# Optimization experiments

Measured on AMD Instinct MI355X. Metric: run time of the kernel, lower is better.

## Reference

```python
import jax, jax.numpy as jnp
import numpy as np

FORMULA_OH_SIZES = [20, 20, 20, 20, 20]
SPECT_BIN_N = 512


def layer_norm(x, g, b, eps=1e-5):
    m = jnp.mean(x, axis=-1, keepdims=True)
    v = jnp.var(x, axis=-1, keepdims=True)
    return (x - m) * jax.lax.rsqrt(v + eps) * g + b


def gru_cell(x, h, W_ih, W_hh, b_ih, b_hh):
    # torch.nn.GRUCell math
    gi = x @ W_ih.T + b_ih
    gh = h @ W_hh.T + b_hh
    i_r, i_z, i_n = jnp.split(gi, 3, axis=-1)
    h_r, h_z, h_n = jnp.split(gh, 3, axis=-1)
    r = jax.nn.sigmoid(i_r + h_r)
    z = jax.nn.sigmoid(i_z + h_z)
    n = jnp.tanh(i_n + r * h_n)
    return (1.0 - z) * n + z * h


def structured_one_hot(x, sizes, accum=True):
    # x: [N, len(sizes)] integer element counts -> concatenated (accumulated) one-hots
    outs = []
    for i, s in enumerate(sizes):
        v = jnp.clip(x[:, i].astype(jnp.int32), 0, s - 1)
        if accum:
            oh = (jnp.arange(s)[None, :] <= v[:, None]).astype(jnp.float32)  # thermometer
        else:
            oh = jax.nn.one_hot(v, s, dtype=jnp.float32)
        outs.append(oh)
    return jnp.concatenate(outs, axis=-1)


def setup_inputs():
    key = jax.random.key(0)
    ks = jax.random.split(key, 16)
    B, A, GF, HW, S, M = 16, 32, 128, 4, 4096, 8
    G = GF * HW                       # 512 = g_feat_in * highway_steps_n
    FE = sum(FORMULA_OH_SIZES)        # 100
    D = 512                           # internal_d
    vert_feat_in = jax.random.normal(ks[0], (B, A, GF, HW), jnp.float32)
    vert_mask_in = jnp.ones((B, A), jnp.float32)
    elem_id = jax.random.randint(ks[1], (B, A), 0, 5)
    vert_element_oh = jax.nn.one_hot(elem_id, 5, dtype=jnp.float32)
    adj_oh = jnp.zeros((B, A, A, 4), jnp.float32)  # unused by forward
    atom_subsets = jax.random.bernoulli(ks[2], 0.5, (B, S, A)).astype(jnp.float32)
    masses = jax.random.uniform(ks[3], (B, S, M), jnp.float32, 0.0, SPECT_BIN_N - 1.0)
    intens = jax.random.uniform(ks[4], (B, S, M), jnp.float32)
    atom_subsets_peaks = jnp.stack([masses, intens], axis=-1)

    def lin(k, o, i):
        return (jax.random.normal(k, (o, i), jnp.float32) / np.sqrt(i)).astype(jnp.float32)

    return dict(
        vert_feat_in=vert_feat_in, vert_mask_in=vert_mask_in,
        vert_element_oh=vert_element_oh, adj_oh=adj_oh,
        atom_subsets=atom_subsets, atom_subsets_peaks=atom_subsets_peaks,
        ln_sub_g=jnp.ones((G,), jnp.float32), ln_sub_b=jnp.zeros((G,), jnp.float32),
        W_ih=lin(ks[5], 3 * G, FE), W_hh=lin(ks[6], 3 * G, G),
        b_ih=jnp.zeros((3 * G,), jnp.float32), b_hh=jnp.zeros((3 * G,), jnp.float32),
        W1=lin(ks[7], D, G), b1=jnp.zeros((D,), jnp.float32),
        W2a=lin(ks[8], D, D), b2a=jnp.zeros((D,), jnp.float32),
        W2b=lin(ks[9], D, D), b2b=jnp.zeros((D,), jnp.float32),
        ln_pre_g=jnp.ones((D,), jnp.float32), ln_pre_b=jnp.zeros((D,), jnp.float32),
        Ws=lin(ks[10], 1, D), bs=jnp.zeros((1,), jnp.float32),
    )


def reference(vert_feat_in, vert_mask_in, vert_element_oh, adj_oh, atom_subsets,
              atom_subsets_peaks, ln_sub_g, ln_sub_b, W_ih, W_hh, b_ih, b_hh,
              W1, b1, W2a, b2a, W2b, b2b, ln_pre_g, ln_pre_b, Ws, bs):
    B, A, GF, HW = vert_feat_in.shape
    S = atom_subsets.shape[1]
    vf = vert_feat_in.reshape(B, A, GF * HW)                       # [B,A,G]
    masked_vf = vf * vert_mask_in[:, :, None]
    subs_m = atom_subsets * vert_mask_in[:, None, :]               # [B,S,A]
    swvs = jnp.einsum('bag,bsa->bsg', masked_vf, subs_m)           # [B,S,G]
    # per-subset element counts -> structured one-hot formula encoding
    counts = jnp.einsum('bae,bsa->bse', vert_element_oh, atom_subsets).astype(jnp.int32)
    pf_flat = structured_one_hot(counts.reshape(B * S, -1), FORMULA_OH_SIZES, accum=True)
    subset_size = jnp.sum(subs_m, axis=2) + 1e-4                   # [B,S]
    mean = swvs / subset_size[:, :, None]
    normed = layer_norm(mean, ln_sub_g, ln_sub_b)                  # [B,S,G]
    h = gru_cell(pf_flat, normed.reshape(B * S, -1), W_ih, W_hh, b_ih, b_hh)
    h = h.reshape(normed.shape)
    x = jax.nn.relu(h @ W1.T + b1)
    x = jax.nn.relu(x @ W2a.T + b2a)
    x = jax.nn.relu(x @ W2b.T + b2b)   # (extra F.relu in original is idempotent)
    x = layer_norm(x, ln_pre_g, ln_pre_b)
    scores = (x @ Ws.T + bs)[..., 0]                               # [B,S]
    probs = jax.nn.softmax(scores, axis=-1)
    # mass histogram: scatter intensity*prob into rounded-mass bins
    masses = atom_subsets_peaks[..., 0]                            # [B,S,M]
    intens = atom_subsets_peaks[..., 1]
    bins = jnp.clip(jnp.round(masses).astype(jnp.int32), 0, SPECT_BIN_N - 1)
    contrib = intens * probs[:, :, None]                           # [B,S,M]
    spect = jnp.zeros((B, SPECT_BIN_N), x.dtype).at[
        jnp.arange(B)[:, None], bins.reshape(B, -1)].add(contrib.reshape(B, -1))
    return (spect, probs)
```

## Files before the change

### kernel.cpp

```cpp
#include <hip/hip_runtime.h>
#include <math.h>

#define B_ 16
#define A_ 32
#define G_ 512
#define S_ 4096
#define M_ 8
#define BS_ 65536
#define KC_ 640
#define NG_ 1536
#define SMH 16384

typedef _Float16 half8 __attribute__((ext_vector_type(8)));
typedef _Float16 half4v __attribute__((ext_vector_type(4)));
typedef _Float16 half2v __attribute__((ext_vector_type(2)));
typedef float floatx4 __attribute__((ext_vector_type(4)));

typedef const __attribute__((address_space(1))) void* gas_t;
typedef __attribute__((address_space(3))) void* las_t;

__device__ __forceinline__ float wave_sum_f(float v){
#pragma unroll
  for (int o = 32; o > 0; o >>= 1) v += __shfl_xor(v, o);
  return v;
}
__device__ __forceinline__ float wave_max_f(float v){
#pragma unroll
  for (int o = 32; o > 0; o >>= 1) v = fmaxf(v, __shfl_xor(v, o));
  return v;
}
__device__ __forceinline__ float sigmoidf_(float x){ return 1.f/(1.f+__expf(-x)); }
__device__ __forceinline__ float tanhf_(float x){ return 1.f - 2.f/(__expf(2.f*x)+1.f); }

__global__ __launch_bounds__(256) void k_cvt3(const float* __restrict__ s0,
                                              const float* __restrict__ s1,
                                              const float* __restrict__ s2,
                                              _Float16* __restrict__ d){
  const float* s = (blockIdx.y == 0) ? s0 : (blockIdx.y == 1) ? s1 : s2;
  int i = (blockIdx.x*256 + threadIdx.x)*4;
  if (i >= G_*G_) return;
  float4 v = *(const float4*)(s+i);
  half4v o; o[0]=(_Float16)v.x; o[1]=(_Float16)v.y; o[2]=(_Float16)v.z; o[3]=(_Float16)v.w;
  *(half4v*)(d + (size_t)blockIdx.y*G_*G_ + i) = o;
}

__global__ __launch_bounds__(64) void k_buildw(const float* __restrict__ Whh,
                                               const float* __restrict__ Wih,
                                               _Float16* __restrict__ Wcat){
  int j = blockIdx.x;
  for (int p = threadIdx.x; p < KC_; p += 64){
    float v = 0.f;
    if (p < 512) v = Whh[(size_t)j*512 + p];
    else if (p < 612) v = Wih[(size_t)j*100 + (p - 512)];
    Wcat[(size_t)j*KC_ + p] = (_Float16)v;
  }
}

__global__ __launch_bounds__(256) void k_prep_mfma(
    const float* __restrict__ vf, const float* __restrict__ mask,
    const float* __restrict__ eoh, const float* __restrict__ subs,
    const float* __restrict__ ln_g, const float* __restrict__ ln_b,
    _Float16* __restrict__ Abuf){
  __shared__ _Float16 s_mvfT[G_*A_];
  __shared__ _Float16 s_sm[128*A_];
  __shared__ float s_m[A_];
  __shared__ float s_e[A_*5];
  __shared__ float s_ssum[128];
  __shared__ float s_red1[2][4][16];
  __shared__ float s_red2[2][4][16];
  int tid = threadIdx.x;
  int bx = blockIdx.x, b = blockIdx.y;
  int lane = tid & 63, w = tid >> 6;
  int q = lane >> 4, l15 = lane & 15;
  size_t row0 = (size_t)b*S_ + (size_t)bx*128;
  if (tid < A_)   s_m[tid] = mask[b*A_ + tid];
  if (tid < A_*5) s_e[tid] = eoh[b*A_*5 + tid];
  __syncthreads();
  {
    int p = tid & 15, gseg = tid >> 4;
    float mk0 = s_m[2*p], mk1 = s_m[2*p+1];
    const float* v0 = vf + ((size_t)b*A_ + 2*p)*G_ + gseg*32;
    const float* v1 = v0 + G_;
#pragma unroll
    for (int i = 0; i < 32; i += 4){
      float4 a = *(const float4*)(v0 + i);
      float4 c = *(const float4*)(v1 + i);
      float av[4] = {a.x, a.y, a.z, a.w};
      float cv[4] = {c.x, c.y, c.z, c.w};
#pragma unroll
      for (int j = 0; j < 4; ++j){
        half2v h; h[0] = (_Float16)(av[j]*mk0); h[1] = (_Float16)(cv[j]*mk1);
        *(half2v*)(s_mvfT + (gseg*32 + i + j)*A_ + 2*p) = h;
      }
    }
  }
  {
    int s = tid >> 1, hh = tid & 1;
    const float* sp = subs + (row0 + s)*A_ + hh*16;
    _Float16* dst = s_sm + s*A_ + hh*16;
#pragma unroll
    for (int i = 0; i < 16; i += 4){
      float4 v = *(const float4*)(sp + i);
      half4v h; h[0]=(_Float16)v.x; h[1]=(_Float16)v.y; h[2]=(_Float16)v.z; h[3]=(_Float16)v.w;
      *(half4v*)(dst + i) = h;
    }
  }
  __syncthreads();
  if (tid < 128){
    int s = tid;
    float ssum = 0.f, c0=0.f, c1=0.f, c2=0.f, c3=0.f, c4=0.f;
#pragma unroll
    for (int a = 0; a < A_; ++a){
      float v = (float)s_sm[s*A_ + a];
      ssum += v * s_m[a];
      c0 += v * s_e[a*5+0]; c1 += v * s_e[a*5+1]; c2 += v * s_e[a*5+2];
      c3 += v * s_e[a*5+3]; c4 += v * s_e[a*5+4];
    }
    int cc[5];
    cc[0] = min(max((int)(c0+0.5f),0),19); cc[1] = min(max((int)(c1+0.5f),0),19);
    cc[2] = min(max((int)(c2+0.5f),0),19); cc[3] = min(max((int)(c3+0.5f),0),19);
    cc[4] = min(max((int)(c4+0.5f),0),19);
    s_ssum[s] = ssum;
    _Float16* dst = Abuf + (row0 + s)*KC_ + 512;
#pragma unroll
    for (int t = 0; t < 16; ++t){
      half8 hv;
#pragma unroll
      for (int u = 0; u < 8; ++u){
        int k = t*8 + u;
        float v = 0.f;
        if (k < 100){ int f = k/20, l = k - f*20; v = (l <= cc[f]) ? 1.f : 0.f; }
        hv[u] = (_Float16)v;
      }
      *(half8*)(dst + t*8) = hv;
    }
  }
  half8 bf[8]; float lng[8], lnb[8];
#pragma unroll
  for (int t = 0; t < 8; ++t){
    int g = w*128 + t*16 + l15;
    bf[t] = *(const half8*)(s_mvfT + g*A_ + q*8);
    lng[t] = ln_g[g]; lnb[t] = ln_b[g];
  }
  __syncthreads();
  for (int gi = 0; gi < 8; ++gi){
    half8 af = *(const half8*)(s_sm + (gi*16 + l15)*A_ + q*8);
    floatx4 c[8];
#pragma unroll
    for (int t = 0; t < 8; ++t){
      floatx4 z = {0.f, 0.f, 0.f, 0.f};
      c[t] = __builtin_amdgcn_mfma_f32_16x16x32_f16(af, bf[t], z, 0, 0, 0);
    }
    float p1[4] = {0.f,0.f,0.f,0.f}, p2[4] = {0.f,0.f,0.f,0.f};
#pragma unroll
    for (int t = 0; t < 8; ++t)
#pragma unroll
      for (int r = 0; r < 4; ++r){ float v = c[t][r]; p1[r] += v; p2[r] += v*v; }
#pragma unroll
    for (int off = 1; off < 16; off <<= 1)
#pragma unroll
      for (int r = 0; r < 4; ++r){
        p1[r] += __shfl_xor(p1[r], off);
        p2[r] += __shfl_xor(p2[r], off);
      }
    int gb = gi & 1;
    if (l15 == 0){
#pragma unroll
      for (int r = 0; r < 4; ++r){ s_red1[gb][w][q*4+r] = p1[r]; s_red2[gb][w][q*4+r] = p2[r]; }
    }
    __syncthreads();
#pragma unroll
    for (int r = 0; r < 4; ++r){
      int sl = gi*16 + q*4 + r;
      int rr = q*4 + r;
      float t1 = s_red1[gb][0][rr] + s_red1[gb][1][rr] + s_red1[gb][2][rr] + s_red1[gb][3][rr];
      float t2 = s_red2[gb][0][rr] + s_red2[gb][1][rr] + s_red2[gb][2][rr] + s_red2[gb][3][rr];
      float inv = 1.f/(s_ssum[sl] + 1e-4f);
      float mu = t1*inv*(1.f/512.f);
      float var = t2*inv*inv*(1.f/512.f) - mu*mu;
      float rs = rsqrtf(var + 1e-5f);
      _Float16* orow = Abuf + (row0 + sl)*KC_;
#pragma unroll
      for (int t = 0; t < 8; ++t){
        float o = (c[t][r]*inv - mu)*rs*lng[t] + lnb[t];
        orow[w*128 + t*16 + l15] = (_Float16)o;
      }
    }
  }
}

#define GSTG_A(T) do{ \
    __builtin_amdgcn_global_load_lds((gas_t)(qA0 + (T)*64),            (las_t)(&gmA[(T)&1][0] + wvid*1024),        16, 0, 0); \
    __builtin_amdgcn_global_load_lds((gas_t)(qA1 + (T)*64),            (las_t)(&gmA[(T)&1][0] + wvid*1024 + 512),  16, 0, 0); \
    __builtin_amdgcn_global_load_lds((gas_t)(qA0 + 128*KC_ + (T)*64),  (las_t)(&gmA[(T)&1][0] + 8192 + wvid*1024), 16, 0, 0); \
    __builtin_amdgcn_global_load_lds((gas_t)(qA1 + 128*KC_ + (T)*64),  (las_t)(&gmA[(T)&1][0] + 8192 + wvid*1024 + 512), 16, 0, 0); \
  }while(0)
#define GSTG_B(T) do{ \
    __builtin_amdgcn_global_load_lds((gas_t)(qB0 + (T)*64), (las_t)(&gmB[(T)&1][0] + wvid*1536),        16, 0, 0); \
    __builtin_amdgcn_global_load_lds((gas_t)(qB1 + (T)*64), (las_t)(&gmB[(T)&1][0] + wvid*1536 + 512),  16, 0, 0); \
    __builtin_amdgcn_global_load_lds((gas_t)(qB2 + (T)*64), (las_t)(&gmB[(T)&1][0] + wvid*1536 + 1024), 16, 0, 0); \
  }while(0)
#define GRD_A(DST, T, MF0) do{ \
    const _Float16* ba_ = &gmA[(T)&1][0]; \
    DST[0][0] = *(const half8*)(ba_ + aoff0 + (MF0)*1024); \
    DST[0][1] = *(const half8*)(ba_ + aoff1 + (MF0)*1024); \
    DST[1][0] = *(const half8*)(ba_ + aoff0 + ((MF0)+1)*1024); \
    DST[1][1] = *(const half8*)(ba_ + aoff1 + ((MF0)+1)*1024); \
  }while(0)
#define GRD_B(DST, T) do{ \
    const _Float16* bb_ = &gmB[(T)&1][0]; \
    _Pragma("unroll") \
    for (int g_ = 0; g_ < 3; ++g_){ \
      DST[g_][0] = *(const half8*)(bb_ + bo0[g_]); \
      DST[g_][1] = *(const half8*)(bb_ + bo1[g_]); \
    } \
  }while(0)
#define GMMQ(AV, BV, MF0, G2) do{ \
    _Pragma("unroll") \
    for (int u_ = 0; u_ < 2; ++u_){ \
      acc[(MF0)+u_][0]  = __builtin_amdgcn_mfma_f32_16x16x32_f16(AV[u_][0], BV[0][0], acc[(MF0)+u_][0], 0, 0, 0); \
      acc[(MF0)+u_][0]  = __builtin_amdgcn_mfma_f32_16x16x32_f16(AV[u_][1], BV[0][1], acc[(MF0)+u_][0], 0, 0, 0); \
      acc[(MF0)+u_][1]  = __builtin_amdgcn_mfma_f32_16x16x32_f16(AV[u_][0], BV[1][0], acc[(MF0)+u_][1], 0, 0, 0); \
      acc[(MF0)+u_][1]  = __builtin_amdgcn_mfma_f32_16x16x32_f16(AV[u_][1], BV[1][1], acc[(MF0)+u_][1], 0, 0, 0); \
      acc[(MF0)+u_][G2] = __builtin_amdgcn_mfma_f32_16x16x32_f16(AV[u_][0], BV[2][0], acc[(MF0)+u_][G2], 0, 0, 0); \
      acc[(MF0)+u_][G2] = __builtin_amdgcn_mfma_f32_16x16x32_f16(AV[u_][1], BV[2][1], acc[(MF0)+u_][G2], 0, 0, 0); \
    } \
  }while(0)
#define GPH0(T, BC, G2) do{ if ((T)+1 <= 9) GSTG_A((T)+1); GRD_A(a_o, T, 2); \
    __builtin_amdgcn_s_barrier(); __builtin_amdgcn_s_setprio(1); GMMQ(a_e, BC, 0, G2); \
    __builtin_amdgcn_s_setprio(0); __builtin_amdgcn_s_barrier(); }while(0)
#define GPH1(T, BC, G2) do{ if ((T)+2 <= 9) GSTG_B((T)+2); GRD_A(a_e, T, 4); \
    __builtin_amdgcn_s_barrier(); __builtin_amdgcn_s_setprio(1); GMMQ(a_o, BC, 2, G2); \
    __builtin_amdgcn_s_setprio(0); __builtin_amdgcn_s_barrier(); }while(0)
#define GPH2(T, BC, G2) do{ GRD_A(a_o, T, 6); \
    __builtin_amdgcn_s_barrier(); __builtin_amdgcn_s_setprio(1); GMMQ(a_e, BC, 4, G2); \
    __builtin_amdgcn_s_setprio(0); __builtin_amdgcn_s_barrier(); }while(0)
#define GPH3(T, BC, BN, G2) do{ \
    if ((T) < 9){ \
      if ((T)+2 <= 9) asm volatile("s_waitcnt vmcnt(3)" ::: "memory"); \
      else            asm volatile("s_waitcnt vmcnt(0)" ::: "memory"); \
      GRD_B(BN, (T)+1); GRD_A(a_e, (T)+1, 0); \
    } \
    __builtin_amdgcn_s_barrier(); __builtin_amdgcn_s_setprio(1); GMMQ(a_o, BC, 6, G2); \
    __builtin_amdgcn_s_setprio(0); __builtin_amdgcn_s_barrier(); }while(0)
#define GTILE(T, BC, BN, G2) do{ GPH0(T, BC, G2); GPH1(T, BC, G2); GPH2(T, BC, G2); GPH3(T, BC, BN, G2); }while(0)

__global__ __launch_bounds__(512, 2) void k_gru8(
    const _Float16* __restrict__ Abuf, const _Float16* __restrict__ Wcat,
    const float* __restrict__ bih, const float* __restrict__ bhh,
    _Float16* __restrict__ H){
  __shared__ _Float16 gmA[2][SMH];
  __shared__ _Float16 gmB[2][192*64];
  int tid = threadIdx.x;
  int lane = tid & 63, wvid = tid >> 6;
  int wm = wvid & 1, wn = wvid >> 1;
  int q = lane >> 4, l15 = lane & 15;
  int x_ = l15 & 7;
  int bid = blockIdx.x;
  int mt = (bid & 7)*32 + (bid >> 6);
  int dt = (bid >> 3) & 7;
  int m0 = mt*256, d0 = dt*64;
  int swzlo = (q ^ (x_ & 3))*8;
  int aoff0 = (wm*128 + l15)*64 + ((0 ^ (x_>>2))*4)*8 + swzlo;
  int aoff1 = (wm*128 + l15)*64 + ((1 ^ (x_>>2))*4)*8 + swzlo;
  int bo0[3], bo1[3];
#pragma unroll
  for (int g = 0; g < 3; ++g){
    int rb = (g*64 + wn*16 + l15)*64;
    bo0[g] = rb + ((0 ^ (x_>>2))*4)*8 + swzlo;
    bo1[g] = rb + ((1 ^ (x_>>2))*4)*8 + swzlo;
  }
  int srow = wvid*16 + (lane >> 3);
  int sc = ((lane & 7) ^ ((lane >> 3) & 7))*8;
  const _Float16* qA0 = Abuf + (size_t)(m0 + srow)*KC_ + sc;
  const _Float16* qA1 = Abuf + (size_t)(m0 + srow + 8)*KC_ + sc;
  int rb0 = wvid*24 + (lane >> 3);
  const _Float16* qB0 = Wcat + (size_t)(((rb0    )>>6)*512 + d0 + ((rb0    )&63))*KC_ + sc;
  const _Float16* qB1 = Wcat + (size_t)(((rb0+ 8)>>6)*512 + d0 + ((rb0+ 8)&63))*KC_ + sc;
  const _Float16* qB2 = Wcat + (size_t)(((rb0+16)>>6)*512 + d0 + ((rb0+16)&63))*KC_ + sc;
  floatx4 acc[8][4] = {};
  half8 a_e[2][2], a_o[2][2], bA[3][2], bB[3][2];
  GSTG_A(0); GSTG_B(0); GSTG_B(1);
  asm volatile("s_waitcnt vmcnt(3)" ::: "memory");
  __builtin_amdgcn_s_barrier();
  GRD_B(bA, 0); GRD_A(a_e, 0, 0);
  GTILE(0, bA, bB, 2); GTILE(1, bB, bA, 2);
  GTILE(2, bA, bB, 2); GTILE(3, bB, bA, 2);
  GTILE(4, bA, bB, 2); GTILE(5, bB, bA, 2);
  GTILE(6, bA, bB, 2); GTILE(7, bB, bA, 2);
  GTILE(8, bA, bB, 3); GTILE(9, bB, bA, 3);
  int d = d0 + wn*16 + l15;
  float br  = bih[d] + bhh[d];
  float bz  = bih[512+d] + bhh[512+d];
  float bnh = bhh[1024+d];
  float bni = bih[1024+d];
#pragma unroll
  for (int mf = 0; mf < 8; ++mf){
#pragma unroll
    for (int r = 0; r < 4; ++r){
      int m = m0 + wm*128 + mf*16 + q*4 + r;
      float gr  = acc[mf][0][r] + br;
      float gz  = acc[mf][1][r] + bz;
      float hn  = acc[mf][2][r] + bnh;
      float in_ = acc[mf][3][r] + bni;
      float rrv = sigmoidf_(gr);
      float zz  = sigmoidf_(gz);
      float nn  = tanhf_(in_ + rrv*hn);
      float hp  = (float)Abuf[(size_t)m*KC_ + d];
      H[(size_t)m*G_ + d] = (_Float16)((1.f-zz)*nn + zz*hp);
    }
  }
}

#define STG_A8(T) do{ \
    __builtin_amdgcn_global_load_lds((gas_t)(pA0 + (T)*64),           (las_t)(&smA8[(T)&1][0] + wvid*1024),        16, 0, 0); \
    __builtin_amdgcn_global_load_lds((gas_t)(pA1 + (T)*64),           (las_t)(&smA8[(T)&1][0] + wvid*1024 + 512),  16, 0, 0); \
    __builtin_amdgcn_global_load_lds((gas_t)(pA0 + 128*G_ + (T)*64),  (las_t)(&smA8[(T)&1][0] + 8192 + wvid*1024), 16, 0, 0); \
    __builtin_amdgcn_global_load_lds((gas_t)(pA1 + 128*G_ + (T)*64),  (las_t)(&smA8[(T)&1][0] + 8192 + wvid*1024 + 512), 16, 0, 0); \
  }while(0)
#define STG_B8(T,H) do{ \
    __builtin_amdgcn_global_load_lds((gas_t)(pB0 + (H)*128*G_ + (T)*64), (las_t)(&smB8[(T)&1][0] + (H)*8192 + wvid*1024),       16, 0, 0); \
    __builtin_amdgcn_global_load_lds((gas_t)(pB1 + (H)*128*G_ + (T)*64), (las_t)(&smB8[(T)&1][0] + (H)*8192 + wvid*1024 + 512), 16, 0, 0); \
  }while(0)
#define RD_A8(DST, T, MF0) do{ \
    const _Float16* ba_ = &smA8[(T)&1][0]; \
    DST[0][0] = *(const half8*)(ba_ + aoff0 + (MF0)*1024); \
    DST[0][1] = *(const half8*)(ba_ + aoff1 + (MF0)*1024); \
    DST[1][0] = *(const half8*)(ba_ + aoff0 + ((MF0)+1)*1024); \
    DST[1][1] = *(const half8*)(ba_ + aoff1 + ((MF0)+1)*1024); \
  }while(0)
#define RD_B8(DST, T) do{ \
    const _Float16* bb_ = &smB8[(T)&1][0]; \
    _Pragma("unroll") \
    for (int nf_ = 0; nf_ < 4; ++nf_){ \
      DST[nf_][0] = *(const half8*)(bb_ + boff0 + nf_*1024); \
      DST[nf_][1] = *(const half8*)(bb_ + boff1 + nf_*1024); \
    } \
  }while(0)
#define MMQ8(AV, BV, MF0) do{ \
    _Pragma("unroll") \
    for (int u_ = 0; u_ < 2; ++u_) \
    _Pragma("unroll") \
    for (int nf_ = 0; nf_ < 4; ++nf_){ \
      acc[(MF0)+u_][nf_] = __builtin_amdgcn_mfma_f32_16x16x32_f16(AV[u_][0], BV[nf_][0], acc[(MF0)+u_][nf_], 0, 0, 0); \
      acc[(MF0)+u_][nf_] = __builtin_amdgcn_mfma_f32_16x16x32_f16(AV[u_][1], BV[nf_][1], acc[(MF0)+u_][nf_], 0, 0, 0); \
    } \
  }while(0)
#define PH_Q0(T, BC) do{ if ((T)+1 <= 7) STG_A8((T)+1); RD_A8(a_o, T, 2); \
    __builtin_amdgcn_s_barrier(); __builtin_amdgcn_s_setprio(1); MMQ8(a_e, BC, 0); \
    __builtin_amdgcn_s_setprio(0); __builtin_amdgcn_s_barrier(); }while(0)
#define PH_Q1(T, BC) do{ if ((T)+2 <= 7) STG_B8((T)+2, 0); RD_A8(a_e, T, 4); \
    __builtin_amdgcn_s_barrier(); __builtin_amdgcn_s_setprio(1); MMQ8(a_o, BC, 2); \
    __builtin_amdgcn_s_setprio(0); __builtin_amdgcn_s_barrier(); }while(0)
#define PH_Q2(T, BC) do{ if ((T)+2 <= 7) STG_B8((T)+2, 1); RD_A8(a_o, T, 6); \
    __builtin_amdgcn_s_barrier(); __builtin_amdgcn_s_setprio(1); MMQ8(a_e, BC, 4); \
    __builtin_amdgcn_s_setprio(0); __builtin_amdgcn_s_barrier(); }while(0)
#define PH_Q3(T, BC, BN) do{ \
    if ((T) < 7){ \
      if ((T) < 6) asm volatile("s_waitcnt vmcnt(4)" ::: "memory"); \
      else         asm volatile("s_waitcnt vmcnt(0)" ::: "memory"); \
      RD_B8(BN, (T)+1); RD_A8(a_e, (T)+1, 0); \
    } \
    __builtin_amdgcn_s_barrier(); __builtin_amdgcn_s_setprio(1); MMQ8(a_o, BC, 6); \
    __builtin_amdgcn_s_setprio(0); __builtin_amdgcn_s_barrier(); }while(0)
#define TILE8(T, BC, BN) do{ PH_Q0(T, BC); PH_Q1(T, BC); PH_Q2(T, BC); PH_Q3(T, BC, BN); }while(0)

#define K8_SETUP(Amat, Wmat) \
  int tid = threadIdx.x; \
  int lane = tid & 63, wvid = tid >> 6; \
  int wm = wvid & 1, wn = wvid >> 1; \
  int q = lane >> 4, l15 = lane & 15; \
  int x_ = l15 & 7; \
  int bid = blockIdx.x; \
  int wg = (bid & 7)*64 + (bid >> 3); \
  int mt = wg >> 1, nt = wg & 1; \
  int m0 = mt*256, n0 = nt*256; \
  int swzlo = (q ^ (x_ & 3))*8; \
  int aoff0 = (wm*128 + l15)*64 + ((0 ^ (x_>>2))*4)*8 + swzlo; \
  int aoff1 = (wm*128 + l15)*64 + ((1 ^ (x_>>2))*4)*8 + swzlo; \
  int boff0 = (wn*64 + l15)*64 + ((0 ^ (x_>>2))*4)*8 + swzlo; \
  int boff1 = (wn*64 + l15)*64 + ((1 ^ (x_>>2))*4)*8 + swzlo; \
  int srow = wvid*16 + (lane >> 3); \
  int sc = ((lane & 7) ^ ((lane >> 3) & 7))*8; \
  const _Float16* pA0 = Amat + (size_t)(m0 + srow)*G_ + sc; \
  const _Float16* pA1 = Amat + (size_t)(m0 + srow + 8)*G_ + sc; \
  const _Float16* pB0 = Wmat + (size_t)(n0 + srow)*G_ + sc; \
  const _Float16* pB1 = Wmat + (size_t)(n0 + srow + 8)*G_ + sc; \
  floatx4 acc[8][4] = {}; \
  half8 a_e[2][2], a_o[2][2], bA[4][2], bB[4][2]; \
  STG_A8(0); STG_B8(0,0); STG_B8(0,1); STG_B8(1,0); STG_B8(1,1); \
  asm volatile("s_waitcnt vmcnt(4)" ::: "memory"); \
  __builtin_amdgcn_s_barrier(); \
  RD_B8(bA, 0); RD_A8(a_e, 0, 0); \
  TILE8(0, bA, bB); TILE8(1, bB, bA); \
  TILE8(2, bA, bB); TILE8(3, bB, bA); \
  TILE8(4, bA, bB); TILE8(5, bB, bA); \
  TILE8(6, bA, bB); TILE8(7, bB, bA);

__global__ __launch_bounds__(512, 2) void k_gemm8(
    const _Float16* __restrict__ A, const _Float16* __restrict__ W,
    const float* __restrict__ bias, _Float16* __restrict__ Out){
  __shared__ _Float16 smA8[2][SMH];
  __shared__ _Float16 smB8[2][SMH];
  K8_SETUP(A, W)
  float bv[4];
#pragma unroll
  for (int nf = 0; nf < 4; ++nf) bv[nf] = bias[n0 + wn*64 + nf*16 + l15];
#pragma unroll
  for (int mf = 0; mf < 8; ++mf){
    int m = m0 + wm*128 + mf*16 + q*4;
#pragma unroll
    for (int nf = 0; nf < 4; ++nf){
      int n = n0 + wn*64 + nf*16 + l15;
#pragma unroll
      for (int r = 0; r < 4; ++r)
        Out[(size_t)(m+r)*G_ + n] = (_Float16)fmaxf(acc[mf][nf][r] + bv[nf], 0.f);
    }
  }
}

__global__ __launch_bounds__(512, 2) void k_ff38(
    const _Float16* __restrict__ A, const _Float16* __restrict__ W,
    const float* __restrict__ bias, const float* __restrict__ ln_pre_g,
    const float* __restrict__ Ws, float* __restrict__ Pbuf){
  __shared__ _Float16 smA8[2][SMH];
  __shared__ _Float16 smB8[2][SMH];
  K8_SETUP(A, W)
  float gws[4], bv[4];
#pragma unroll
  for (int nf = 0; nf < 4; ++nf){
    int n = n0 + wn*64 + nf*16 + l15;
    gws[nf] = ln_pre_g[n]*Ws[n];
    bv[nf] = bias[n];
  }
  float* sP = (float*)&smB8[0][0];
#pragma unroll
  for (int mf = 0; mf < 8; ++mf){
#pragma unroll
    for (int r = 0; r < 4; ++r){
      float p1 = 0.f, p2 = 0.f, p3 = 0.f;
#pragma unroll
      for (int nf = 0; nf < 4; ++nf){
        float xv = fmaxf(acc[mf][nf][r] + bv[nf], 0.f);
        p1 += xv; p2 += xv*xv; p3 += gws[nf]*xv;
      }
#pragma unroll
      for (int off = 1; off < 16; off <<= 1){
        p1 += __shfl_xor(p1, off);
        p2 += __shfl_xor(p2, off);
        p3 += __shfl_xor(p3, off);
      }
      if (l15 == 0){
        int rl = wm*128 + mf*16 + q*4 + r;
        sP[(rl*4 + wn)*3 + 0] = p1;
        sP[(rl*4 + wn)*3 + 1] = p2;
        sP[(rl*4 + wn)*3 + 2] = p3;
      }
    }
  }
  __syncthreads();
  if (tid < 256){
    int m = m0 + tid;
    float* dst = Pbuf + ((size_t)m*2 + nt)*3;
#pragma unroll
    for (int c = 0; c < 3; ++c)
      dst[c] = sP[(tid*4+0)*3+c] + sP[(tid*4+1)*3+c] +
               sP[(tid*4+2)*3+c] + sP[(tid*4+3)*3+c];
  }
}

__global__ __launch_bounds__(256) void k_score_fin(
    const float* __restrict__ Pbuf, const float* __restrict__ g,
    const float* __restrict__ bta, const float* __restrict__ Ws,
    const float* __restrict__ bs, float* __restrict__ scores,
    float* __restrict__ spect){
  __shared__ float red[8];
  int tid = threadIdx.x, lane = tid & 63, wv = tid >> 6;
  if (blockIdx.x < 32) spect[(size_t)blockIdx.x*256 + tid] = 0.f;
  int i0 = tid*2;
  float c1p = g[i0]*Ws[i0] + g[i0+1]*Ws[i0+1];
  float c2p = bta[i0]*Ws[i0] + bta[i0+1]*Ws[i0+1];
  c1p = wave_sum_f(c1p); c2p = wave_sum_f(c2p);
  if (lane == 0){ red[wv] = c1p; red[4+wv] = c2p; }
  __syncthreads();
  float c1 = red[0]+red[1]+red[2]+red[3];
  float c2 = red[4]+red[5]+red[6]+red[7] + bs[0];
  size_t row = (size_t)blockIdx.x*256 + tid;
  const float* p = Pbuf + row*6;
  float2 u0 = *(const float2*)p;
  float2 u1 = *(const float2*)(p+2);
  float2 u2 = *(const float2*)(p+4);
  float P1 = u0.x + u1.y;
  float P2 = u0.y + u2.x;
  float P3 = u1.x + u2.y;
  float mu = P1*(1.f/512.f);
  float var = P2*(1.f/512.f) - mu*mu;
  float rs = rsqrtf(var + 1e-5f);
  scores[row] = rs*(P3 - mu*c1) + c2;
}

__global__ __launch_bounds__(256) void k_softmax(
    const float* __restrict__ scores, float* __restrict__ probs){
  __shared__ float red[4];
  int b = blockIdx.x, tid = threadIdx.x, lane = tid & 63, wv = tid >> 6;
  const float* sp = scores + (size_t)b*S_;
  float* pp = probs + (size_t)b*S_;
  float mx = -1e30f;
  for (int i = tid; i < S_; i += 256) mx = fmaxf(mx, sp[i]);
  mx = wave_max_f(mx);
  if (lane == 0) red[wv] = mx;
  __syncthreads();
  mx = fmaxf(fmaxf(red[0], red[1]), fmaxf(red[2], red[3]));
  __syncthreads();
  float sum = 0.f;
  for (int i = tid; i < S_; i += 256){
    float e = __expf(sp[i]-mx);
    pp[i] = e;
    sum += e;
  }
  sum = wave_sum_f(sum);
  if (lane == 0) red[wv] = sum;
  __syncthreads();
  sum = red[0]+red[1]+red[2]+red[3];
  float inv = 1.f/sum;
  for (int i = tid; i < S_; i += 256)
    pp[i] *= inv;
}

__global__ __launch_bounds__(256) void k_spect_p(
    const float* __restrict__ peaks, const float* __restrict__ probs,
    float* __restrict__ spect){
  __shared__ float bins[512];
  int b = blockIdx.x, chunk = blockIdx.y, tid = threadIdx.x;
  bins[tid] = 0.f; bins[tid+256] = 0.f;
  __syncthreads();
  int s0 = chunk*(S_/8);
  for (int i = tid; i < (S_/8)*M_; i += 256){
    int s = s0 + (i >> 3), m = i & 7;
    const float* pk = peaks + (((size_t)b*S_ + s)*M_ + m)*2;
    float mass = pk[0], inten = pk[1];
    float p = probs[(size_t)b*S_ + s];
    int bin = (int)rintf(mass);
    bin = min(max(bin, 0), 511);
    atomicAdd(&bins[bin], inten*p);
  }
  __syncthreads();
  atomicAdd(&spect[(size_t)b*512 + tid],       bins[tid]);
  atomicAdd(&spect[(size_t)b*512 + tid + 256], bins[tid+256]);
}

extern "C" void kernel_launch(void* const* d_in, const int* in_sizes, int n_in,
                              void* d_out, int out_size, void* d_ws, size_t ws_size,
                              hipStream_t stream) {
  const float* vf       = (const float*)d_in[0];
  const float* mask     = (const float*)d_in[1];
  const float* eoh      = (const float*)d_in[2];
  const float* subs     = (const float*)d_in[4];
  const float* peaks    = (const float*)d_in[5];
  const float* ln_sub_g = (const float*)d_in[6];
  const float* ln_sub_b = (const float*)d_in[7];
  const float* W_ih     = (const float*)d_in[8];
  const float* W_hh     = (const float*)d_in[9];
  const float* b_ih     = (const float*)d_in[10];
  const float* b_hh     = (const float*)d_in[11];
  const float* W1       = (const float*)d_in[12];
  const float* b1       = (const float*)d_in[13];
  const float* W2a      = (const float*)d_in[14];
  const float* b2a      = (const float*)d_in[15];
  const float* W2b      = (const float*)d_in[16];
  const float* b2b      = (const float*)d_in[17];
  const float* ln_pre_g = (const float*)d_in[18];
  const float* ln_pre_b = (const float*)d_in[19];
  const float* Ws       = (const float*)d_in[20];
  const float* bs       = (const float*)d_in[21];
  float* out = (float*)d_out;
  float* probs_out = out + (size_t)B_*512;

  char* w = (char*)d_ws;
  float* scores = (float*)w;     w += (size_t)BS_*4;
  float* Pbuf   = (float*)w;     w += (size_t)BS_*12*4;
  _Float16* Wcat = (_Float16*)w; w += (size_t)NG_*KC_*2;
  _Float16* W1h  = (_Float16*)w; w += (size_t)G_*G_*2;
  _Float16* W2ah = (_Float16*)w; w += (size_t)G_*G_*2;
  _Float16* W2bh = (_Float16*)w; w += (size_t)G_*G_*2;
  _Float16* Abuf = (_Float16*)w; w += (size_t)BS_*KC_*2;
  _Float16* bufh0 = (_Float16*)w;
  _Float16* bufh1 = Abuf;

  k_cvt3<<<dim3((G_*G_/4+255)/256, 3), 256, 0, stream>>>(W1, W2a, W2b, W1h);
  k_buildw<<<NG_, 64, 0, stream>>>(W_hh, W_ih, Wcat);
  k_prep_mfma<<<dim3(S_/128, B_), 256, 0, stream>>>(vf, mask, eoh, subs,
                                                    ln_sub_g, ln_sub_b, Abuf);
  k_gru8<<<2048, 512, 0, stream>>>(Abuf, Wcat, b_ih, b_hh, bufh0);
  k_gemm8<<<512, 512, 0, stream>>>(bufh0, W1h,  b1,  bufh1);
  k_gemm8<<<512, 512, 0, stream>>>(bufh1, W2ah, b2a, bufh0);
  k_ff38<<<512, 512, 0, stream>>>(bufh0, W2bh, b2b, ln_pre_g, Ws, Pbuf);
  k_score_fin<<<BS_/256, 256, 0, stream>>>(Pbuf, ln_pre_g, ln_pre_b, Ws, bs,
                                           scores, out);
  k_softmax<<<B_, 256, 0, stream>>>(scores, probs_out);
  k_spect_p<<<dim3(B_, 8), 256, 0, stream>>>(peaks, probs_out, out);
}
```

Measured before the change: 465.9 us.

## Replace four-phase barrier-pipelined GRU GEMM schedule with simple per-tile sync loop

Drops the hand-interleaved four-phase schedule in the GRU GEMM main loop, which used split barriers, priority raises, explicit vmcnt waits and a two-deep register double buffer for B fragments. Each K tile now does one __syncthreads, issues the async staging of the next A and B tiles, then reads all fragments from LDS and runs the MFMAs in order. This removes many barriers and one set of B registers. In exchange it loses the fine-grained overlap of LDS reads with MFMAs, and it may expose more global-load latency at each tile's sync.

```diff
diff --git a/kernel.cpp b/kernel.cpp
--- a/kernel.cpp
+++ b/kernel.cpp
@@ -226,24 +226,15 @@
       acc[(MF0)+u_][G2] = __builtin_amdgcn_mfma_f32_16x16x32_f16(AV[u_][1], BV[2][1], acc[(MF0)+u_][G2], 0, 0, 0); \
     } \
   }while(0)
-#define GPH0(T, BC, G2) do{ if ((T)+1 <= 9) GSTG_A((T)+1); GRD_A(a_o, T, 2); \
-    __builtin_amdgcn_s_barrier(); __builtin_amdgcn_s_setprio(1); GMMQ(a_e, BC, 0, G2); \
-    __builtin_amdgcn_s_setprio(0); __builtin_amdgcn_s_barrier(); }while(0)
-#define GPH1(T, BC, G2) do{ if ((T)+2 <= 9) GSTG_B((T)+2); GRD_A(a_e, T, 4); \
-    __builtin_amdgcn_s_barrier(); __builtin_amdgcn_s_setprio(1); GMMQ(a_o, BC, 2, G2); \
-    __builtin_amdgcn_s_setprio(0); __builtin_amdgcn_s_barrier(); }while(0)
-#define GPH2(T, BC, G2) do{ GRD_A(a_o, T, 6); \
-    __builtin_amdgcn_s_barrier(); __builtin_amdgcn_s_setprio(1); GMMQ(a_e, BC, 4, G2); \
-    __builtin_amdgcn_s_setprio(0); __builtin_amdgcn_s_barrier(); }while(0)
-#define GPH3(T, BC, BN, G2) do{ \
-    if ((T) < 9){ \
-      if ((T)+2 <= 9) asm volatile("s_waitcnt vmcnt(3)" ::: "memory"); \
-      else            asm volatile("s_waitcnt vmcnt(0)" ::: "memory"); \
-      GRD_B(BN, (T)+1); GRD_A(a_e, (T)+1, 0); \
-    } \
-    __builtin_amdgcn_s_barrier(); __builtin_amdgcn_s_setprio(1); GMMQ(a_o, BC, 6, G2); \
-    __builtin_amdgcn_s_setprio(0); __builtin_amdgcn_s_barrier(); }while(0)
-#define GTILE(T, BC, BN, G2) do{ GPH0(T, BC, G2); GPH1(T, BC, G2); GPH2(T, BC, G2); GPH3(T, BC, BN, G2); }while(0)
+#define GTILE3(T, G2) do{ \
+    __syncthreads(); \
+    if ((T) < 9){ GSTG_A((T)+1); GSTG_B((T)+1); } \
+    GRD_B(bA, T); \
+    GRD_A(a_e, T, 0); GMMQ(a_e, bA, 0, G2); \
+    GRD_A(a_o, T, 2); GMMQ(a_o, bA, 2, G2); \
+    GRD_A(a_e, T, 4); GMMQ(a_e, bA, 4, G2); \
+    GRD_A(a_o, T, 6); GMMQ(a_o, bA, 6, G2); \
+  }while(0)
 
 __global__ __launch_bounds__(512, 2) void k_gru8(
     const _Float16* __restrict__ Abuf, const _Float16* __restrict__ Wcat,
@@ -279,16 +270,13 @@
   const _Float16* qB1 = Wcat + (size_t)(((rb0+ 8)>>6)*512 + d0 + ((rb0+ 8)&63))*KC_ + sc;
   const _Float16* qB2 = Wcat + (size_t)(((rb0+16)>>6)*512 + d0 + ((rb0+16)&63))*KC_ + sc;
   floatx4 acc[8][4] = {};
-  half8 a_e[2][2], a_o[2][2], bA[3][2], bB[3][2];
-  GSTG_A(0); GSTG_B(0); GSTG_B(1);
-  asm volatile("s_waitcnt vmcnt(3)" ::: "memory");
-  __builtin_amdgcn_s_barrier();
-  GRD_B(bA, 0); GRD_A(a_e, 0, 0);
-  GTILE(0, bA, bB, 2); GTILE(1, bB, bA, 2);
-  GTILE(2, bA, bB, 2); GTILE(3, bB, bA, 2);
-  GTILE(4, bA, bB, 2); GTILE(5, bB, bA, 2);
-  GTILE(6, bA, bB, 2); GTILE(7, bB, bA, 2);
-  GTILE(8, bA, bB, 3); GTILE(9, bB, bA, 3);
+  half8 a_e[2][2], a_o[2][2], bA[3][2];
+  GSTG_A(0); GSTG_B(0);
+  GTILE3(0, 2); GTILE3(1, 2);
+  GTILE3(2, 2); GTILE3(3, 2);
+  GTILE3(4, 2); GTILE3(5, 2);
+  GTILE3(6, 2); GTILE3(7, 2);
+  GTILE3(8, 3); GTILE3(9, 3);
   int d = d0 + wn*16 + l15;
   float br  = bih[d] + bhh[d];
   float bz  = bih[512+d] + bhh[512+d];
```

Measured after the change: 484.2 us. +3.9%, slower.
